# Optimization experiments

Hardware: AMD Instinct MI355X
Metric: run time of the kernel (lower is better)

Reference implementation:

```python
import jax, jax.numpy as jnp
import numpy as np

N_HEADS = 16
WINDOW = 256  # window_size; keep keys with |i-j| <= WINDOW//2


def setup_inputs() -> dict:
    key = jax.random.key(0)
    ks = jax.random.split(key, 6)
    B, S, D = 2, 2048, 1024
    x = jax.random.normal(ks[0], (B, S, D), dtype=jnp.float32)
    # torch nn.Linear weights are [out_features, in_features]
    scale = 1.0 / np.sqrt(D)
    Wq = jax.random.normal(ks[1], (D, D), dtype=jnp.float32) * scale
    Wk = jax.random.normal(ks[2], (D, D), dtype=jnp.float32) * scale
    Wv = jax.random.normal(ks[3], (D, D), dtype=jnp.float32) * scale
    Wo = jax.random.normal(ks[4], (D, D), dtype=jnp.float32) * scale
    # standard ALiBi slopes: 2^(-8*(h+1)/H)
    slopes = jnp.asarray(2.0 ** (-8.0 * (np.arange(1, N_HEADS + 1) / N_HEADS)), dtype=jnp.float32)
    return {"x": x, "Wq": Wq, "Wk": Wk, "Wv": Wv, "Wo": Wo, "slopes": slopes}


def reference(x, Wq, Wk, Wv, Wo, slopes):
    B, S, D = x.shape
    H = N_HEADS
    dk = D // H
    # projections (torch Linear: y = x @ W.T)
    q = jnp.einsum('bsd,od->bso', x, Wq).reshape(B, S, H, dk)
    k = jnp.einsum('bsd,od->bso', x, Wk).reshape(B, S, H, dk)
    v = jnp.einsum('bsd,od->bso', x, Wv).reshape(B, S, H, dk)
    # full score matrix [B,H,S,S]
    scores = jnp.einsum('bqhd,bkhd->bhqk', q, k) / jnp.sqrt(jnp.asarray(dk, x.dtype))
    pos = jnp.arange(S)
    rel = (pos[:, None] - pos[None, :]).astype(x.dtype)          # [S,S] q_pos - k_pos
    scores = scores + slopes[None, :, None, None] * rel[None, None]
    window_mask = jnp.abs(pos[:, None] - pos[None, :]) <= (WINDOW // 2)  # [S,S]
    scores = jnp.where(window_mask[None, None], scores, -jnp.inf)
    attn = jax.nn.softmax(scores, axis=-1)
    out = jnp.einsum('bhqk,bkhd->bqhd', attn, v).reshape(B, S, D)
    return jnp.einsum('bsd,od->bso', out, Wo)
```

## Files before the change

kernel.cpp:

```cpp
#include <hip/hip_runtime.h>
#include <hip/hip_bf16.h>

#define S_LEN   2048
#define D_MODEL 1024
#define NH      16
#define DK      64
#define BATCH   2
#define M_ROWS  (BATCH * S_LEN)
#define LDP     72
#define LDV     66
#define LDW     132

typedef __attribute__((ext_vector_type(8))) short bf16x8;
typedef __attribute__((ext_vector_type(4))) float f32x4;
typedef __attribute__((ext_vector_type(16))) float f32x16;
typedef __attribute__((ext_vector_type(8))) unsigned short us8;
typedef __attribute__((ext_vector_type(4))) unsigned short us4;

static __device__ __forceinline__ unsigned short f2bf(float f) {
    unsigned u = __builtin_bit_cast(unsigned, f);
    u += 0x7fffu + ((u >> 16) & 1u);
    return (unsigned short)(u >> 16);
}

__global__ __launch_bounds__(256) void cvt_all(const float* __restrict__ x,
                                               const float* __restrict__ wq,
                                               const float* __restrict__ wk,
                                               const float* __restrict__ wv,
                                               const float* __restrict__ wo,
                                               unsigned short* __restrict__ dst) {
    const int b = blockIdx.x;
    if (b < 2048) {
        const size_t o8 = (size_t)b * 256 + threadIdx.x;
        const float4* s = (const float4*)x + o8 * 2;
        float4 a = s[0], bb = s[1];
        us8 o;
        o[0] = f2bf(a.x);  o[1] = f2bf(a.y);  o[2] = f2bf(a.z);  o[3] = f2bf(a.w);
        o[4] = f2bf(bb.x); o[5] = f2bf(bb.y); o[6] = f2bf(bb.z); o[7] = f2bf(bb.w);
        *((us8*)dst + o8) = o;
    } else {
        const int wi = (b - 2048) >> 9;
        const float* src = (wi == 0) ? wq : (wi == 1) ? wk : (wi == 2) ? wv : wo;
        const size_t local = (size_t)((b - 2048) & 511) * 256 + threadIdx.x;
        const float4* s = (const float4*)src + local * 2;
        float4 a = s[0], bb = s[1];
        us8 o;
        o[0] = f2bf(a.x);  o[1] = f2bf(a.y);  o[2] = f2bf(a.z);  o[3] = f2bf(a.w);
        o[4] = f2bf(bb.x); o[5] = f2bf(bb.y); o[6] = f2bf(bb.z); o[7] = f2bf(bb.w);
        *((us8*)dst + 524288 + (size_t)wi * 131072 + local) = o;
    }
}

template <int STORE_BF16, int BN>
__global__ __launch_bounds__(256) void mfma_gemm_bt(const unsigned short* __restrict__ A,
                                                    const unsigned short* __restrict__ W,
                                                    void* __restrict__ Cv, int N) {
    constexpr int K = 1024, BM = 128, BK = 64;
    constexpr int MI = (BN == 128) ? 2 : 1;
    constexpr int SMEM = (STORE_BF16 && BN == 128) ? (128 * LDW)
                                                   : (BM * BK + BN * BK);
    __shared__ unsigned short smem[SMEM];
    unsigned short* As = smem;
    unsigned short* Bs = smem + BM * BK;

    const int tid  = threadIdx.x;
    const int w    = tid >> 6;
    const int lane = tid & 63;

    const int nwg = gridDim.x * gridDim.y;
    const int lin = blockIdx.y * gridDim.x + blockIdx.x;
    const int l   = (lin & 7) * (nwg >> 3) + (lin >> 3);
    const int m0 = (l / gridDim.x) * BM;
    const int n0 = (l % gridDim.x) * BN;

    const int wr = (BN == 128) ? (w >> 1) * 64 : w * 32;
    const int wc = (BN == 128) ? (w & 1) * 64 : 0;

    const int srow   = lane >> 3;
    const int schunk = ((lane & 7) ^ (lane >> 3)) * 8;
    const int l31   = lane & 31;
    const int khalf = lane >> 5;
    const int sw    = lane & 7;
    int roff[4];
#pragma unroll
    for (int s = 0; s < 4; ++s)
        roff[s] = ((2 * s + khalf) ^ sw) * 8;

    f32x16 acc[MI][2] = {};

    for (int k0 = 0; k0 < K; k0 += BK) {
        __syncthreads();
#pragma unroll
        for (int t = 0; t < 4; ++t) {
            const int rbase = w * 32 + t * 8;
            const unsigned short* ga = A + (size_t)(m0 + rbase + srow) * K + k0 + schunk;
            __builtin_amdgcn_global_load_lds(
                (const __attribute__((address_space(1))) void*)ga,
                (__attribute__((address_space(3))) void*)(As + rbase * BK), 16, 0, 0);
        }
#pragma unroll
        for (int t = 0; t < BN / 32; ++t) {
            const int rbase = w * (BN / 4) + t * 8;
            const unsigned short* gb = W + (size_t)(n0 + rbase + srow) * K + k0 + schunk;
            __builtin_amdgcn_global_load_lds(
                (const __attribute__((address_space(1))) void*)gb,
                (__attribute__((address_space(3))) void*)(Bs + rbase * BK), 16, 0, 0);
        }
        __syncthreads();

#pragma unroll
        for (int s = 0; s < 4; ++s) {
            bf16x8 af[MI], bfr[2];
#pragma unroll
            for (int i = 0; i < MI; ++i)
                af[i] = *(const bf16x8*)(As + (wr + i * 32 + l31) * BK + roff[s]);
#pragma unroll
            for (int j = 0; j < 2; ++j)
                bfr[j] = *(const bf16x8*)(Bs + (wc + j * 32 + l31) * BK + roff[s]);
#pragma unroll
            for (int i = 0; i < MI; ++i)
#pragma unroll
                for (int j = 0; j < 2; ++j)
                    acc[i][j] = __builtin_amdgcn_mfma_f32_32x32x16_bf16(af[i], bfr[j], acc[i][j], 0, 0, 0);
        }
    }

    if constexpr (STORE_BF16 && BN == 128) {
        __syncthreads();
#pragma unroll
        for (int i = 0; i < 2; ++i)
#pragma unroll
            for (int j = 0; j < 2; ++j)
#pragma unroll
                for (int r = 0; r < 16; ++r) {
                    const int row_l = wr + i * 32 + (r & 3) + 8 * (r >> 2) + 4 * khalf;
                    const int col_l = wc + j * 32 + l31;
                    smem[row_l * LDW + col_l] = f2bf(acc[i][j][r]);
                }
        __syncthreads();
#pragma unroll
        for (int e = 0; e < 8; ++e) {
            const int idx = e * 256 + tid;
            const int row = idx >> 4;
            const int cc  = (idx & 15) * 8;
            us4 lo = *(const us4*)(smem + row * LDW + cc);
            us4 hi = *(const us4*)(smem + row * LDW + cc + 4);
            us8 v;
            v[0] = lo[0]; v[1] = lo[1]; v[2] = lo[2]; v[3] = lo[3];
            v[4] = hi[0]; v[5] = hi[1]; v[6] = hi[2]; v[7] = hi[3];
            *(us8*)((unsigned short*)Cv + (size_t)(m0 + row) * N + n0 + cc) = v;
        }
    } else {
#pragma unroll
        for (int i = 0; i < MI; ++i)
#pragma unroll
            for (int j = 0; j < 2; ++j)
#pragma unroll
                for (int r = 0; r < 16; ++r) {
                    const int gm = m0 + wr + i * 32 + (r & 3) + 8 * (r >> 2) + 4 * khalf;
                    const int gn = n0 + wc + j * 32 + l31;
                    if (STORE_BF16)
                        ((unsigned short*)Cv)[(size_t)gm * N + gn] = f2bf(acc[i][j][r]);
                    else
                        ((float*)Cv)[(size_t)gm * N + gn] = acc[i][j][r];
                }
    }
}

__global__ __launch_bounds__(256) void attn_mfma(const unsigned short* __restrict__ qkvb,
                                                 const float* __restrict__ slopes,
                                                 unsigned short* __restrict__ aoutb) {
    __shared__ unsigned short QPs[64 * LDP];
    __shared__ unsigned short Ks[2 * 64 * 64];
    __shared__ unsigned short Vt[64 * LDV];

    const int tid  = threadIdx.x;
    const int w    = tid >> 6;
    const int lane = tid & 63;

    const int lin = blockIdx.x + 32 * (blockIdx.y + 16 * blockIdx.z);
    const int l   = (lin & 7) * 128 + (lin >> 3);
    const int q0 = (l & 31) * 64;
    const int h  = (l >> 5) & 15;
    const int b  = l >> 9;

    const float slope = slopes[h];
    const size_t rowbase = (size_t)b * S_LEN * 3072;

#pragma unroll
    for (int e = 0; e < 2; ++e) {
        int idx = e * 256 + tid;
        int r = idx >> 3, cc = (idx & 7) * 8;
        us8 v = *(const us8*)(qkvb + rowbase + (size_t)(q0 + r) * 3072 + h * DK + cc);
        *(us8*)(QPs + r * LDP + cc) = v;
    }

    const int col = lane & 15;
    const int rq  = (lane >> 4) * 4;
    const int wq  = w * 16;
    const int fo  = (lane >> 4) * 8;

    const int srowK   = lane >> 3;
    const int schunkK = ((lane & 7) ^ srowK) * 8;
    const int kc0 = (((lane >> 4) + 0) ^ (lane & 7)) * 8;
    const int kc1 = (((lane >> 4) + 4) ^ (lane & 7)) * 8;

    const unsigned short* kbase  = qkvb + rowbase + 1024 + h * DK;
    const unsigned short* vbase0 = qkvb + rowbase + 2048 + h * DK;

    const int rp  = tid >> 3;
    const int ccv = (tid & 7) * 8;

    float qa[4];
#pragma unroll
    for (int r = 0; r < 4; ++r) {
        const int qpos = q0 + wq + rq + r;
        qa[r] = slope * (float)(qpos > 128 ? qpos - 128 : 0) - 12.0f;
    }

    f32x4 o_acc[4] = {};
    float l_part[4] = {0.f, 0.f, 0.f, 0.f};

    {
        const int k0 = q0 - 128;
#pragma unroll
        for (int t = 0; t < 2; ++t) {
            const int rbase = w * 16 + t * 8;
            const unsigned short* gk = kbase + (long long)(k0 + rbase + srowK) * 3072 + schunkK;
            __builtin_amdgcn_global_load_lds(
                (const __attribute__((address_space(1))) void*)gk,
                (__attribute__((address_space(3))) void*)(Ks + rbase * 64), 16, 0, 0);
        }
        const long long kp0 = (long long)(k0 + rp * 2);
        us8 v0 = *(const us8*)(vbase0 + ccv + kp0 * 3072);
        us8 v1 = *(const us8*)(vbase0 + ccv + (kp0 + 1) * 3072);
#pragma unroll
        for (int t = 0; t < 8; ++t) {
            unsigned pk = (unsigned)(unsigned short)v0[t] | ((unsigned)(unsigned short)v1[t] << 16);
            *(unsigned*)(Vt + (ccv + t) * LDV + rp * 2) = pk;
        }
    }
    __syncthreads();

    const bf16x8 aq0 = *(const bf16x8*)(QPs + (wq + col) * LDP + fo);
    const bf16x8 aq1 = *(const bf16x8*)(QPs + (wq + col) * LDP + fo + 32);

    int cur = 0;
    for (int c = 0; c < 5; ++c) {
        const int k0 = q0 - 128 + c * 64;
        const unsigned short* KsC = Ks + cur * 4096;
        const bool have_next = (c < 4);

        us8 nv0, nv1;
        if (have_next) {
            const int kn0 = k0 + 64;
            unsigned short* KsN = (unsigned short*)Ks + (cur ^ 1) * 4096;
#pragma unroll
            for (int t = 0; t < 2; ++t) {
                const int rbase = w * 16 + t * 8;
                const unsigned short* gk = kbase + (long long)(kn0 + rbase + srowK) * 3072 + schunkK;
                __builtin_amdgcn_global_load_lds(
                    (const __attribute__((address_space(1))) void*)gk,
                    (__attribute__((address_space(3))) void*)(KsN + rbase * 64), 16, 0, 0);
            }
            const long long kp0 = (long long)(kn0 + rp * 2);
            nv0 = *(const us8*)(vbase0 + ccv + kp0 * 3072);
            nv1 = *(const us8*)(vbase0 + ccv + (kp0 + 1) * 3072);
        }

        f32x4 sacc[4] = {};
        __builtin_amdgcn_s_setprio(1);
#pragma unroll
        for (int j = 0; j < 4; ++j) {
            const int tt  = wq - 64 * c - 16 * j;
            const int klo = k0 + 16 * j;
            const bool any_v = (tt <= 0) && (tt >= -256) && (klo < S_LEN) && (klo + 15 >= 0);
            if (any_v) {
                bf16x8 bk0 = *(const bf16x8*)(KsC + (j * 16 + col) * 64 + kc0);
                bf16x8 bk1 = *(const bf16x8*)(KsC + (j * 16 + col) * 64 + kc1);
                sacc[j] = __builtin_amdgcn_mfma_f32_16x16x32_bf16(aq0, bk0, sacc[j], 0, 0, 0);
                sacc[j] = __builtin_amdgcn_mfma_f32_16x16x32_bf16(aq1, bk1, sacc[j], 0, 0, 0);
            }
        }
        __builtin_amdgcn_s_setprio(0);

#pragma unroll
        for (int j = 0; j < 4; ++j) {
            const int tt  = wq - 64 * c - 16 * j;
            const int klo = k0 + 16 * j;
            const bool any_v = (tt <= 0) && (tt >= -256) && (klo < S_LEN) && (klo + 15 >= 0);
            unsigned short* ps = QPs + (wq + rq) * LDP + j * 16 + col;
            if (!any_v) {
#pragma unroll
                for (int r = 0; r < 4; ++r) ps[r * LDP] = 0;
            } else {
                const float kb = slope * (float)(klo + col);
                const bool all_v = (tt <= -16) && (tt >= -240) && (klo >= 0) && (klo + 15 < S_LEN);
                if (all_v) {
#pragma unroll
                    for (int r = 0; r < 4; ++r) {
                        float p = __expf(fmaf(sacc[j][r], 0.125f, qa[r] - kb));
                        l_part[r] += p;
                        ps[r * LDP] = f2bf(p);
                    }
                } else {
                    const int kpos = klo + col;
                    const bool kin = (unsigned)kpos < (unsigned)S_LEN;
#pragma unroll
                    for (int r = 0; r < 4; ++r) {
                        const int rel = (q0 + wq + rq + r) - kpos;
                        const bool ok = kin && (rel <= 128) && (rel >= -128);
                        float p = 0.f;
                        if (ok) p = __expf(fmaf(sacc[j][r], 0.125f, qa[r] - kb));
                        l_part[r] += p;
                        ps[r * LDP] = f2bf(p);
                    }
                }
            }
        }

        {
            bf16x8 ap0 = *(const bf16x8*)(QPs + (wq + col) * LDP + fo);
            bf16x8 ap1 = *(const bf16x8*)(QPs + (wq + col) * LDP + fo + 32);
            __builtin_amdgcn_s_setprio(1);
#pragma unroll
            for (int j = 0; j < 4; ++j) {
                bf16x8 bv0 = *(const bf16x8*)(Vt + (j * 16 + col) * LDV + fo);
                bf16x8 bv1 = *(const bf16x8*)(Vt + (j * 16 + col) * LDV + fo + 32);
                o_acc[j] = __builtin_amdgcn_mfma_f32_16x16x32_bf16(ap0, bv0, o_acc[j], 0, 0, 0);
                o_acc[j] = __builtin_amdgcn_mfma_f32_16x16x32_bf16(ap1, bv1, o_acc[j], 0, 0, 0);
            }
            __builtin_amdgcn_s_setprio(0);
        }

        if (have_next) {
            __syncthreads();
#pragma unroll
            for (int t = 0; t < 8; ++t) {
                unsigned pk = (unsigned)(unsigned short)nv0[t] | ((unsigned)(unsigned short)nv1[t] << 16);
                *(unsigned*)(Vt + (ccv + t) * LDV + rp * 2) = pk;
            }
            __syncthreads();
        }
        cur ^= 1;
    }

    float inv[4];
#pragma unroll
    for (int r = 0; r < 4; ++r) {
        float l2 = l_part[r];
#pragma unroll
        for (int off = 1; off < 16; off <<= 1) l2 += __shfl_xor(l2, off, 64);
        inv[r] = 1.f / l2;
    }

#pragma unroll
    for (int j = 0; j < 4; ++j)
#pragma unroll
        for (int r = 0; r < 4; ++r) {
            const int qpos = q0 + wq + rq + r;
            aoutb[((size_t)b * S_LEN + qpos) * D_MODEL + h * DK + j * 16 + col] =
                f2bf(o_acc[j][r] * inv[r]);
        }
}

extern "C" void kernel_launch(void* const* d_in, const int* in_sizes, int n_in,
                              void* d_out, int out_size, void* d_ws, size_t ws_size,
                              hipStream_t stream) {
    const float* x      = (const float*)d_in[0];
    const float* Wq     = (const float*)d_in[1];
    const float* Wk     = (const float*)d_in[2];
    const float* Wv     = (const float*)d_in[3];
    const float* Wo     = (const float*)d_in[4];
    const float* slopes = (const float*)d_in[5];
    float* out = (float*)d_out;

    unsigned short* xb    = (unsigned short*)d_ws;
    unsigned short* wb    = xb    + (size_t)M_ROWS * D_MODEL;
    unsigned short* wob   = wb    + (size_t)3072 * D_MODEL;
    unsigned short* qkvb  = wob   + (size_t)1024 * D_MODEL;
    unsigned short* aoutb = qkvb  + (size_t)M_ROWS * 3072;

    dim3 blk(256);
    cvt_all<<<4096, blk, 0, stream>>>(x, Wq, Wk, Wv, Wo, xb);
    mfma_gemm_bt<1, 128><<<dim3(3072 / 128, M_ROWS / 128), blk, 0, stream>>>(xb, wb, qkvb, 3072);
    attn_mfma<<<dim3(S_LEN / 64, NH, BATCH), blk, 0, stream>>>(qkvb, slopes, aoutb);
    mfma_gemm_bt<0, 64><<<dim3(1024 / 64, M_ROWS / 128), blk, 0, stream>>>(aoutb, wob, out, 1024);
}
```

Baseline: 150.5 us.

## Use two-wave 128x128 QKV GEMM with larger per-wave MFMA tiles

Adds a dedicated QKV projection kernel that runs 128 threads (two waves) per 128x128 tile instead of 256. Each wave computes a 64x128 sub-tile with 2x4 32x32x16 bf16 MFMAs, which raises fragment reuse from LDS per MFMA. Tiles are loaded straight into LDS with global_load_lds and an XOR swizzle, and output goes through an LDS-staged bf16 store. The kernel keeps 128 accumulators per lane, so occupancy and latency hiding may drop, and there is no double buffering.

After: 170.8 us. 1.13x slower.

```diff
diff --git a/kernel.cpp b/kernel.cpp
--- a/kernel.cpp
+++ b/kernel.cpp
@@ -51,6 +51,99 @@
     }
 }
 
+__global__ __launch_bounds__(128) void gemm_qkv_w2(const unsigned short* __restrict__ A,
+                                                   const unsigned short* __restrict__ W,
+                                                   unsigned short* __restrict__ C) {
+    constexpr int K = 1024, BM = 128, BN = 128, BK = 64;
+    __shared__ unsigned short smem[128 * LDW];
+    unsigned short* As = smem;
+    unsigned short* Bs = smem + BM * BK;
+
+    const int tid  = threadIdx.x;
+    const int w    = tid >> 6;
+    const int lane = tid & 63;
+
+    const int nwg = gridDim.x * gridDim.y;
+    const int lin = blockIdx.y * gridDim.x + blockIdx.x;
+    const int l   = (lin & 7) * (nwg >> 3) + (lin >> 3);
+    const int m0 = (l / gridDim.x) * BM;
+    const int n0 = (l % gridDim.x) * BN;
+
+    const int srow   = lane >> 3;
+    const int schunk = ((lane & 7) ^ srow) * 8;
+    const int l31    = lane & 31;
+    const int khalf  = lane >> 5;
+    const int sw     = lane & 7;
+    int roff[4];
+#pragma unroll
+    for (int s = 0; s < 4; ++s)
+        roff[s] = ((2 * s + khalf) ^ sw) * 8;
+
+    f32x16 acc[2][4] = {};
+
+    for (int k0 = 0; k0 < K; k0 += BK) {
+        __syncthreads();
+#pragma unroll
+        for (int t = 0; t < 8; ++t) {
+            const int rbase = w * 64 + t * 8;
+            const unsigned short* ga = A + (size_t)(m0 + rbase + srow) * K + k0 + schunk;
+            __builtin_amdgcn_global_load_lds(
+                (const __attribute__((address_space(1))) void*)ga,
+                (__attribute__((address_space(3))) void*)(As + rbase * BK), 16, 0, 0);
+        }
+#pragma unroll
+        for (int t = 0; t < 8; ++t) {
+            const int rbase = w * 64 + t * 8;
+            const unsigned short* gb = W + (size_t)(n0 + rbase + srow) * K + k0 + schunk;
+            __builtin_amdgcn_global_load_lds(
+                (const __attribute__((address_space(1))) void*)gb,
+                (__attribute__((address_space(3))) void*)(Bs + rbase * BK), 16, 0, 0);
+        }
+        __syncthreads();
+
+#pragma unroll
+        for (int s = 0; s < 4; ++s) {
+            bf16x8 af[2], bfr[4];
+#pragma unroll
+            for (int i = 0; i < 2; ++i)
+                af[i] = *(const bf16x8*)(As + (w * 64 + i * 32 + l31) * BK + roff[s]);
+#pragma unroll
+            for (int j = 0; j < 4; ++j)
+                bfr[j] = *(const bf16x8*)(Bs + (j * 32 + l31) * BK + roff[s]);
+#pragma unroll
+            for (int i = 0; i < 2; ++i)
+#pragma unroll
+                for (int j = 0; j < 4; ++j)
+                    acc[i][j] = __builtin_amdgcn_mfma_f32_32x32x16_bf16(af[i], bfr[j], acc[i][j], 0, 0, 0);
+        }
+    }
+
+    __syncthreads();
+#pragma unroll
+    for (int i = 0; i < 2; ++i)
+#pragma unroll
+        for (int j = 0; j < 4; ++j)
+#pragma unroll
+            for (int r = 0; r < 16; ++r) {
+                const int row_l = w * 64 + i * 32 + (r & 3) + 8 * (r >> 2) + 4 * khalf;
+                const int col_l = j * 32 + l31;
+                smem[row_l * LDW + col_l] = f2bf(acc[i][j][r]);
+            }
+    __syncthreads();
+#pragma unroll
+    for (int e = 0; e < 16; ++e) {
+        const int idx = e * 128 + tid;
+        const int row = idx >> 4;
+        const int cc  = (idx & 15) * 8;
+        us4 lo = *(const us4*)(smem + row * LDW + cc);
+        us4 hi = *(const us4*)(smem + row * LDW + cc + 4);
+        us8 v;
+        v[0] = lo[0]; v[1] = lo[1]; v[2] = lo[2]; v[3] = lo[3];
+        v[4] = hi[0]; v[5] = hi[1]; v[6] = hi[2]; v[7] = hi[3];
+        *(us8*)(C + (size_t)(m0 + row) * 3072 + n0 + cc) = v;
+    }
+}
+
 template <int STORE_BF16, int BN>
 __global__ __launch_bounds__(256) void mfma_gemm_bt(const unsigned short* __restrict__ A,
                                                     const unsigned short* __restrict__ W,
@@ -383,7 +476,7 @@
 
     dim3 blk(256);
     cvt_all<<<4096, blk, 0, stream>>>(x, Wq, Wk, Wv, Wo, xb);
-    mfma_gemm_bt<1, 128><<<dim3(3072 / 128, M_ROWS / 128), blk, 0, stream>>>(xb, wb, qkvb, 3072);
+    gemm_qkv_w2<<<dim3(3072 / 128, M_ROWS / 128), dim3(128), 0, stream>>>(xb, wb, qkvb);
     attn_mfma<<<dim3(S_LEN / 64, NH, BATCH), blk, 0, stream>>>(qkvb, slopes, aoutb);
     mfma_gemm_bt<0, 64><<<dim3(1024 / 64, M_ROWS / 128), blk, 0, stream>>>(aoutb, wob, out, 1024);
 }
```
